# Kernel tuning notes

Hardware: AMD Instinct MI355X
Metric: run time of the kernel (lower is better)

The kernel has to match this reference:

```python
import jax, jax.numpy as jnp
import numpy as np

B, CH, N = 8, 256, 2048


def setup_inputs() -> dict:
    key = jax.random.key(0)
    kk, kq, kv = jax.random.split(key, 3)
    k = jax.random.normal(kk, (B, CH, N), dtype=jnp.float32)
    q = jax.random.normal(kq, (B, N, CH), dtype=jnp.float32)
    v = jax.random.normal(kv, (B, N, CH), dtype=jnp.float32)
    return {"k": k, "q": q, "v": v}


def reference(k, q, v):
    # 'embedded' mode: attn = softmax(ch^-0.5 * q @ k), dropout p=0 is identity
    ch = k.shape[1]
    scale = ch ** (-0.5)
    attn = jax.nn.softmax(scale * jnp.einsum('bnc,bcm->bnm', q, k), axis=-1)  # [B, N, N]
    attended = jnp.einsum('bnm,bmc->bnc', attn, v)  # [B, N, CH]
    return jnp.transpose(attended, (0, 2, 1))  # [B, CH, N]
```

## Files before the change

kernel.cpp:

```cpp
#include <hip/hip_runtime.h>

namespace {

constexpr int kB = 8;
constexpr int kCH = 256;
constexpr int kN = 2048;
constexpr int NSPLIT = 2;
constexpr int SLICE = kN / NSPLIT;
constexpr int KVC = 64;
constexpr int NWAVE = 8;
constexpr int QBLK = 128;
constexpr int PS_STRIDE = KVC + 8;

constexpr float SCALE = 0.0625f;
constexpr float LOG2E = 1.4426950408889634f;
constexpr float DEFER_THR = 4.0f;

typedef _Float16 f16x8 __attribute__((ext_vector_type(8)));
typedef _Float16 f16x4 __attribute__((ext_vector_type(4)));
typedef float f32x4 __attribute__((ext_vector_type(4)));

__device__ __forceinline__ void gload_lds16(const void* g, void* l) {
  __builtin_amdgcn_global_load_lds(
      (const __attribute__((address_space(1))) void*)g,
      (__attribute__((address_space(3))) void*)l, 16, 0, 0);
}

__global__ __launch_bounds__(256) void transpose_both(
    const float* __restrict__ kin, const float* __restrict__ vin,
    _Float16* __restrict__ kt, _Float16* __restrict__ vt) {
  __shared__ _Float16 T[64][72];
  const bool isV = blockIdx.z >= 8;
  const int b = isV ? blockIdx.z - 8 : blockIdx.z;
  const int R = isV ? kN : kCH, C = isV ? kCH : kN;
  const int r0 = (isV ? blockIdx.x : blockIdx.y) * 64;
  const int c0 = (isV ? blockIdx.y : blockIdx.x) * 64;
  const float* in = isV ? vin : kin;
  _Float16* out = isV ? vt : kt;
  const int t = threadIdx.x;

  const float* ib =
      in + (size_t)b * R * C + (size_t)(r0 + (t >> 2)) * C + c0 + (t & 3) * 4;
#pragma unroll
  for (int q = 0; q < 4; ++q) {
    f32x4 v = *(const f32x4*)(ib + q * 16);
    f16x4 w;
    w[0] = (_Float16)v[0]; w[1] = (_Float16)v[1];
    w[2] = (_Float16)v[2]; w[3] = (_Float16)v[3];
    *(f16x4*)(&T[t >> 2][(t & 3) * 4 + q * 16]) = w;
  }
  __syncthreads();
  const int cl = t >> 2, ch = t & 3;
  f16x8 o0, o1;
#pragma unroll
  for (int j = 0; j < 8; ++j) o0[j] = T[ch * 16 + j][cl];
#pragma unroll
  for (int j = 0; j < 8; ++j) o1[j] = T[ch * 16 + 8 + j][cl];
  _Float16* ob = out + (size_t)b * R * C + (size_t)(c0 + cl) * R + r0 + ch * 16;
  *(f16x8*)(ob) = o0;
  *(f16x8*)(ob + 8) = o1;
}

__global__ __launch_bounds__(512, 1) void attn_part(
    const _Float16* __restrict__ kt, const float* __restrict__ qg,
    const _Float16* __restrict__ vt, _Float16* __restrict__ pacc,
    float* __restrict__ pm, float* __restrict__ pl)
{
  __shared__ alignas(16) char KsB[2][64 * 512];
  __shared__ alignas(16) char VsB[2][256 * 128];
  __shared__ alignas(16) _Float16 Ps[NWAVE][16][PS_STRIDE];
  __shared__ float red[NWAVE][16];

  const int tid = threadIdx.x;
  const int wv = tid >> 6;
  const int lane = tid & 63;
  const int s = lane & 15;
  const int qd = lane >> 4;
  const int sw = (s & 7) << 4;
  const int qd16 = qd << 4;

  const int bg = blockIdx.x & 15;
  const int qt = blockIdx.x >> 4;
  const int b = bg >> 1, g = bg & 1;
  const int n0w = qt * QBLK + wv * 16;
  const int kvb = g * SLICE;

  const char* ktB = (const char*)(kt + (size_t)b * kN * kCH);
  const char* vtB = (const char*)(vt + (size_t)b * kCH * kN);
  const float* qb = qg + (size_t)b * kN * kCH;

  f16x8 qf[8];
  {
    const float* qrow = qb + (size_t)(n0w + s) * kCH + qd * 8;
#pragma unroll
    for (int ks = 0; ks < 8; ++ks) {
      f32x4 a = *(const f32x4*)(qrow + ks * 32);
      f32x4 c = *(const f32x4*)(qrow + ks * 32 + 4);
      f16x8 h;
      h[0] = (_Float16)a[0]; h[1] = (_Float16)a[1];
      h[2] = (_Float16)a[2]; h[3] = (_Float16)a[3];
      h[4] = (_Float16)c[0]; h[5] = (_Float16)c[1];
      h[6] = (_Float16)c[2]; h[7] = (_Float16)c[3];
      qf[ks] = h;
    }
  }

  f32x4 acc[16];
#pragma unroll
  for (int i = 0; i < 16; ++i) acc[i] = f32x4{0.f, 0.f, 0.f, 0.f};
  float m_r[4] = {-1e30f, -1e30f, -1e30f, -1e30f};
  float l_r[4] = {0.f, 0.f, 0.f, 0.f};

  auto STAGE = [&](int bf, int kv0) {
    const char* kSrc = ktB + (size_t)kv0 * 512;
    const char* vSrc = vtB + (size_t)kv0 * 2;
    char* kDst = KsB[bf];
    char* vDst = VsB[bf];
#pragma unroll
    for (int ii = 0; ii < 4; ++ii) {
      const int j = ii * 8 + wv;
      const int L = j * 1024 + lane * 16;
      {
        const int row = L >> 9, cb = L & 511;
        gload_lds16(kSrc + (size_t)(row << 9) + (cb ^ ((row & 7) << 4)),
                    kDst + j * 1024);
      }
      {
        const int row = L >> 7, cb = L & 127;
        gload_lds16(vSrc + (size_t)row * 4096 + (cb ^ ((row & 7) << 4)),
                    vDst + j * 1024);
      }
    }
  };

  constexpr int NCHUNK = SLICE / KVC;
  STAGE(0, kvb);
  __syncthreads();

  for (int ck = 0; ck < NCHUNK; ++ck) {
    const int cur = ck & 1;
    if (ck + 1 < NCHUNK) STAGE(cur ^ 1, kvb + (ck + 1) * KVC);

    f32x4 sacc[4];
#pragma unroll
    for (int mc = 0; mc < 4; ++mc) sacc[mc] = f32x4{0.f, 0.f, 0.f, 0.f};
#pragma unroll
    for (int mc = 0; mc < 4; ++mc) {
      const char* kr = KsB[cur] + (mc * 16 + s) * 512;
#pragma unroll
      for (int ks = 0; ks < 8; ++ks) {
        f16x8 bf = *(const f16x8*)(kr + (((ks << 6) | qd16) ^ sw));
        sacc[mc] = __builtin_amdgcn_mfma_f32_16x16x32_f16(qf[ks], bf, sacc[mc], 0, 0, 0);
      }
    }

    float pmax[4];
#pragma unroll
    for (int r = 0; r < 4; ++r)
      pmax[r] = fmaxf(fmaxf(sacc[0][r], sacc[1][r]), fmaxf(sacc[2][r], sacc[3][r]));
#pragma unroll
    for (int off = 1; off < 16; off <<= 1) {
#pragma unroll
      for (int r = 0; r < 4; ++r)
        pmax[r] = fmaxf(pmax[r], __shfl_xor(pmax[r], off, 64));
    }

    bool grow = false;
#pragma unroll
    for (int r = 0; r < 4; ++r)
      grow = grow || (SCALE * pmax[r] > m_r[r] + DEFER_THR);
    if (__any((int)grow)) {
      float corr[4];
#pragma unroll
      for (int r = 0; r < 4; ++r) {
        float mn = fmaxf(m_r[r], SCALE * pmax[r]);
        corr[r] = exp2f((m_r[r] - mn) * LOG2E);
        m_r[r] = mn;
        l_r[r] *= corr[r];
      }
      if (s == 0) {
#pragma unroll
        for (int r = 0; r < 4; ++r) red[wv][qd * 4 + r] = corr[r];
      }
      asm volatile("s_waitcnt lgkmcnt(0)" ::: "memory");
      const float sc = red[wv][s];
#pragma unroll
      for (int i = 0; i < 16; ++i) acc[i] *= sc;
    }

    float lsum[4] = {0.f, 0.f, 0.f, 0.f};
#pragma unroll
    for (int mc = 0; mc < 4; ++mc) {
#pragma unroll
      for (int r = 0; r < 4; ++r) {
        float pvf = exp2f((SCALE * sacc[mc][r] - m_r[r]) * LOG2E);
        lsum[r] += pvf;
        Ps[wv][qd * 4 + r][mc * 16 + s] = (_Float16)pvf;
      }
    }
#pragma unroll
    for (int off = 1; off < 16; off <<= 1) {
#pragma unroll
      for (int r = 0; r < 4; ++r) lsum[r] += __shfl_xor(lsum[r], off, 64);
    }
#pragma unroll
    for (int r = 0; r < 4; ++r) l_r[r] += lsum[r];

    asm volatile("s_waitcnt lgkmcnt(0)" ::: "memory");

#pragma unroll
    for (int ms = 0; ms < 2; ++ms) {
      f16x8 pf = *(const f16x8*)(&Ps[wv][s][ms * 32 + qd * 8]);
#pragma unroll
      for (int ct = 0; ct < 16; ++ct) {
        const char* vr = VsB[cur] + (ct * 16 + s) * 128;
        f16x8 vf = *(const f16x8*)(vr + (((ms << 6) | qd16) ^ sw));
        acc[ct] = __builtin_amdgcn_mfma_f32_16x16x32_f16(vf, pf, acc[ct], 0, 0, 0);
      }
    }
    __syncthreads();
  }

  _Float16* pb = pacc + (size_t)(b * NSPLIT + g) * kCH * kN;
#pragma unroll
  for (int ct = 0; ct < 16; ++ct) {
#pragma unroll
    for (int r = 0; r < 4; ++r) {
      const int c = ct * 16 + qd * 4 + r;
      pb[(size_t)c * kN + n0w + s] = (_Float16)acc[ct][r];
    }
  }
  if (s == 0) {
#pragma unroll
    for (int r = 0; r < 4; ++r) {
      const int n = n0w + qd * 4 + r;
      pm[((size_t)b * kN + n) * NSPLIT + g] = m_r[r];
      pl[((size_t)b * kN + n) * NSPLIT + g] = l_r[r];
    }
  }
}

__global__ void attn_merge(const _Float16* __restrict__ pacc,
                           const float* __restrict__ pm,
                           const float* __restrict__ pl,
                           float* __restrict__ out) {
  const int b = blockIdx.z;
  const int c = blockIdx.y * 16 + (threadIdx.x >> 4);
  const int nn0 = blockIdx.x * 256 + (threadIdx.x & 15) * 16;

  f16x8 dA[NSPLIT], dB[NSPLIT];
#pragma unroll
  for (int g = 0; g < NSPLIT; ++g) {
    const _Float16* p = pacc + ((size_t)(b * NSPLIT + g) * kCH + c) * kN + nn0;
    dA[g] = *(const f16x8*)(p);
    dB[g] = *(const f16x8*)(p + 8);
  }
  float mv[32], lv[32];
  const float* pmB = pm + ((size_t)b * kN + nn0) * NSPLIT;
  const float* plB = pl + ((size_t)b * kN + nn0) * NSPLIT;
#pragma unroll
  for (int q = 0; q < 8; ++q) {
    *(f32x4*)&mv[q * 4] = *(const f32x4*)(pmB + q * 4);
    *(f32x4*)&lv[q * 4] = *(const f32x4*)(plB + q * 4);
  }
  float res[16];
#pragma unroll
  for (int j = 0; j < 16; ++j) {
    float m0 = mv[2 * j], m1 = mv[2 * j + 1];
    float M = fmaxf(m0, m1);
    float a0 = exp2f((m0 - M) * LOG2E);
    float a1 = exp2f((m1 - M) * LOG2E);
    float L = a0 * lv[2 * j] + a1 * lv[2 * j + 1];
    float v = (j < 8) ? a0 * (float)dA[0][j] + a1 * (float)dA[1][j]
                      : a0 * (float)dB[0][j - 8] + a1 * (float)dB[1][j - 8];
    res[j] = v / L;
  }
  float* o = out + ((size_t)b * kCH + c) * kN + nn0;
#pragma unroll
  for (int j = 0; j < 4; ++j)
    *(f32x4*)(o + j * 4) = f32x4{res[j * 4], res[j * 4 + 1], res[j * 4 + 2], res[j * 4 + 3]};
}

constexpr int QBLK_FB = 64;
constexpr int KVBLK_FB = 64;
constexpr int KS_STRIDE_FB = kCH + 8;
constexpr int VS_STRIDE_FB = KVBLK_FB + 8;

__global__ __launch_bounds__(256, 1) void attn_fwd_fb(
    const float* __restrict__ kg, const float* __restrict__ qg,
    const float* __restrict__ vg, float* __restrict__ og)
{
  __shared__ alignas(16) _Float16 Ks[KVBLK_FB][KS_STRIDE_FB];
  __shared__ alignas(16) _Float16 Vs[kCH][VS_STRIDE_FB];
  __shared__ alignas(16) _Float16 Psf[4][16][VS_STRIDE_FB];
  __shared__ float red[4][16];

  const int tid = threadIdx.x;
  const int wv = tid >> 6, lane = tid & 63, s = lane & 15, qd = lane >> 4;
  const int b = blockIdx.x & 7, qt = blockIdx.x >> 3;
  const int n0w = qt * QBLK_FB + wv * 16;
  const float* kb = kg + (size_t)b * kCH * kN;
  const float* qb = qg + (size_t)b * kN * kCH;
  const float* vb = vg + (size_t)b * kN * kCH;
  float* ob = og + (size_t)b * kCH * kN;

  f16x8 qf[8];
  {
    const float* qrow = qb + (size_t)(n0w + s) * kCH + qd * 8;
#pragma unroll
    for (int ks = 0; ks < 8; ++ks) {
      f32x4 a = *(const f32x4*)(qrow + ks * 32);
      f32x4 c = *(const f32x4*)(qrow + ks * 32 + 4);
      f16x8 h;
      h[0] = (_Float16)a[0]; h[1] = (_Float16)a[1];
      h[2] = (_Float16)a[2]; h[3] = (_Float16)a[3];
      h[4] = (_Float16)c[0]; h[5] = (_Float16)c[1];
      h[6] = (_Float16)c[2]; h[7] = (_Float16)c[3];
      qf[ks] = h;
    }
  }
  f32x4 acc[16];
#pragma unroll
  for (int i = 0; i < 16; ++i) acc[i] = f32x4{0.f, 0.f, 0.f, 0.f};
  float m_r[4] = {-1e30f, -1e30f, -1e30f, -1e30f};
  float l_r[4] = {0.f, 0.f, 0.f, 0.f};

  for (int kv0 = 0; kv0 < kN; kv0 += KVBLK_FB) {
    __syncthreads();
    {
      const int m0 = 4 * (tid >> 4), c0b = 4 * (tid & 15);
#pragma unroll
      for (int p = 0; p < 4; ++p) {
        const int c0 = c0b + 64 * p;
        const float* src = kb + (size_t)c0 * kN + kv0 + m0;
        f32x4 r0 = *(const f32x4*)(src);
        f32x4 r1 = *(const f32x4*)(src + kN);
        f32x4 r2 = *(const f32x4*)(src + 2 * kN);
        f32x4 r3 = *(const f32x4*)(src + 3 * kN);
#pragma unroll
        for (int i = 0; i < 4; ++i) {
          f16x4 w;
          w[0] = (_Float16)r0[i]; w[1] = (_Float16)r1[i];
          w[2] = (_Float16)r2[i]; w[3] = (_Float16)r3[i];
          *(f16x4*)(&Ks[m0 + i][c0]) = w;
        }
      }
    }
    {
      const int m0 = 4 * (tid & 15), c0b = 4 * (tid >> 4);
#pragma unroll
      for (int p = 0; p < 4; ++p) {
        const int c0 = c0b + 64 * p;
        const float* src = vb + (size_t)(kv0 + m0) * kCH + c0;
        f32x4 r0 = *(const f32x4*)(src);
        f32x4 r1 = *(const f32x4*)(src + kCH);
        f32x4 r2 = *(const f32x4*)(src + 2 * kCH);
        f32x4 r3 = *(const f32x4*)(src + 3 * kCH);
#pragma unroll
        for (int i = 0; i < 4; ++i) {
          f16x4 w;
          w[0] = (_Float16)r0[i]; w[1] = (_Float16)r1[i];
          w[2] = (_Float16)r2[i]; w[3] = (_Float16)r3[i];
          *(f16x4*)(&Vs[c0 + i][m0]) = w;
        }
      }
    }
    __syncthreads();

    f32x4 sacc[4];
#pragma unroll
    for (int mc = 0; mc < 4; ++mc) sacc[mc] = f32x4{0.f, 0.f, 0.f, 0.f};
#pragma unroll
    for (int mc = 0; mc < 4; ++mc) {
#pragma unroll
      for (int ks = 0; ks < 8; ++ks) {
        f16x8 bf = *(const f16x8*)(&Ks[mc * 16 + s][ks * 32 + qd * 8]);
        sacc[mc] = __builtin_amdgcn_mfma_f32_16x16x32_f16(qf[ks], bf, sacc[mc], 0, 0, 0);
      }
    }
    float pmax[4];
#pragma unroll
    for (int r = 0; r < 4; ++r)
      pmax[r] = fmaxf(fmaxf(sacc[0][r], sacc[1][r]), fmaxf(sacc[2][r], sacc[3][r]));
#pragma unroll
    for (int off = 1; off < 16; off <<= 1) {
#pragma unroll
      for (int r = 0; r < 4; ++r)
        pmax[r] = fmaxf(pmax[r], __shfl_xor(pmax[r], off, 64));
    }
    float corr[4], lsum[4];
#pragma unroll
    for (int r = 0; r < 4; ++r) {
      float mn = fmaxf(m_r[r], SCALE * pmax[r]);
      corr[r] = exp2f((m_r[r] - mn) * LOG2E);
      m_r[r] = mn;
      lsum[r] = 0.f;
    }
#pragma unroll
    for (int mc = 0; mc < 4; ++mc) {
#pragma unroll
      for (int r = 0; r < 4; ++r) {
        float pvf = exp2f((SCALE * sacc[mc][r] - m_r[r]) * LOG2E);
        lsum[r] += pvf;
        Psf[wv][qd * 4 + r][mc * 16 + s] = (_Float16)pvf;
      }
    }
#pragma unroll
    for (int off = 1; off < 16; off <<= 1) {
#pragma unroll
      for (int r = 0; r < 4; ++r) lsum[r] += __shfl_xor(lsum[r], off, 64);
    }
#pragma unroll
    for (int r = 0; r < 4; ++r) l_r[r] = l_r[r] * corr[r] + lsum[r];
    if (s == 0) {
#pragma unroll
      for (int r = 0; r < 4; ++r) red[wv][qd * 4 + r] = corr[r];
    }
    asm volatile("s_waitcnt lgkmcnt(0)" ::: "memory");
    const float sc = red[wv][s];
#pragma unroll
    for (int i = 0; i < 16; ++i) acc[i] *= sc;
#pragma unroll
    for (int ms = 0; ms < 2; ++ms) {
      f16x8 pf = *(const f16x8*)(&Psf[wv][s][ms * 32 + qd * 8]);
#pragma unroll
      for (int ct = 0; ct < 16; ++ct) {
        f16x8 vf = *(const f16x8*)(&Vs[ct * 16 + s][ms * 32 + qd * 8]);
        acc[ct] = __builtin_amdgcn_mfma_f32_16x16x32_f16(vf, pf, acc[ct], 0, 0, 0);
      }
    }
  }
  if (s == 0) {
#pragma unroll
    for (int r = 0; r < 4; ++r) red[wv][qd * 4 + r] = 1.0f / l_r[r];
  }
  asm volatile("s_waitcnt lgkmcnt(0)" ::: "memory");
  const float inv = red[wv][s];
#pragma unroll
  for (int ct = 0; ct < 16; ++ct) {
#pragma unroll
    for (int r = 0; r < 4; ++r) {
      const int c = ct * 16 + qd * 4 + r;
      ob[(size_t)c * kN + n0w + s] = acc[ct][r] * inv;
    }
  }
}

constexpr size_t KT_ELEMS = (size_t)kB * kN * kCH;
constexpr size_t PACC_ELEMS = (size_t)NSPLIT * kB * kCH * kN;
constexpr size_t PM_ELEMS = (size_t)kB * kN * NSPLIT;
constexpr size_t WS_NEED =
    (2 * KT_ELEMS + PACC_ELEMS) * sizeof(_Float16) + 2 * PM_ELEMS * sizeof(float);

}

extern "C" void kernel_launch(void* const* d_in, const int* in_sizes, int n_in,
                              void* d_out, int out_size, void* d_ws, size_t ws_size,
                              hipStream_t stream) {
  (void)in_sizes; (void)n_in; (void)out_size;
  const float* k = (const float*)d_in[0];
  const float* q = (const float*)d_in[1];
  const float* v = (const float*)d_in[2];
  float* out = (float*)d_out;

  if (ws_size < WS_NEED) {
    hipLaunchKernelGGL(attn_fwd_fb, dim3(kB * (kN / QBLK_FB)), dim3(256), 0, stream,
                       k, q, v, out);
    return;
  }

  _Float16* kt = (_Float16*)d_ws;
  _Float16* vt = kt + KT_ELEMS;
  _Float16* pacc = vt + KT_ELEMS;
  float* pm = (float*)(pacc + PACC_ELEMS);
  float* pl = pm + PM_ELEMS;

  hipLaunchKernelGGL(transpose_both, dim3(kN / 64, kCH / 64, 16), dim3(256), 0,
                     stream, k, v, kt, vt);
  hipLaunchKernelGGL(attn_part, dim3(kB * (kN / QBLK) * NSPLIT), dim3(512), 0,
                     stream, kt, q, vt, pacc, pm, pl);
  hipLaunchKernelGGL(attn_merge, dim3(kN / 256, kCH / 16, kB), dim3(256), 0, stream,
                     pacc, pm, pl, out);
}
```

Before: 174.1 us.

## Switch attention to 32x32 MFMA with register-resident P and four-way KV split

Rewrites the main attention kernel around 32x32x16 MFMA tiles. Each wave now owns 32 query rows, and S is computed transposed so the P tile stays in registers, repacked with cvt_pkrtz and permlane32_swap instead of being staged through LDS. The KV dimension is split four ways and blocks are allowed two per CU, and the merge kernel now combines four partials. The transpose kernel drops its shared-memory stage and writes f16x4 directly. The aim is to remove the LDS round trip for P and the cross-lane reductions and to raise occupancy, at the cost of more register pressure and more partial-output traffic.

```diff
diff --git a/kernel.cpp b/kernel.cpp
--- a/kernel.cpp
+++ b/kernel.cpp
@@ -1,24 +1,26 @@
 #include <hip/hip_runtime.h>
+#include <stdint.h>
 
 namespace {
 
 constexpr int kB = 8;
 constexpr int kCH = 256;
 constexpr int kN = 2048;
-constexpr int NSPLIT = 2;
+constexpr int NSPLIT = 4;
 constexpr int SLICE = kN / NSPLIT;
 constexpr int KVC = 64;
-constexpr int NWAVE = 8;
-constexpr int QBLK = 128;
-constexpr int PS_STRIDE = KVC + 8;
+constexpr int NCHUNK = SLICE / KVC;
+constexpr int QBLK = 256;
 
 constexpr float SCALE = 0.0625f;
 constexpr float LOG2E = 1.4426950408889634f;
-constexpr float DEFER_THR = 4.0f;
+constexpr float THR = 4.0f;
 
 typedef _Float16 f16x8 __attribute__((ext_vector_type(8)));
 typedef _Float16 f16x4 __attribute__((ext_vector_type(4)));
 typedef float f32x4 __attribute__((ext_vector_type(4)));
+typedef float f32x16 __attribute__((ext_vector_type(16)));
+typedef unsigned int u32x4 __attribute__((ext_vector_type(4)));
 
 __device__ __forceinline__ void gload_lds16(const void* g, void* l) {
   __builtin_amdgcn_global_load_lds(
@@ -29,65 +31,267 @@
 __global__ __launch_bounds__(256) void transpose_both(
     const float* __restrict__ kin, const float* __restrict__ vin,
     _Float16* __restrict__ kt, _Float16* __restrict__ vt) {
-  __shared__ _Float16 T[64][72];
   const bool isV = blockIdx.z >= 8;
-  const int b = isV ? blockIdx.z - 8 : blockIdx.z;
+  const int b = isV ? (int)blockIdx.z - 8 : (int)blockIdx.z;
   const int R = isV ? kN : kCH, C = isV ? kCH : kN;
-  const int r0 = (isV ? blockIdx.x : blockIdx.y) * 64;
-  const int c0 = (isV ? blockIdx.y : blockIdx.x) * 64;
+  const int r0 = (isV ? (int)blockIdx.x : (int)blockIdx.y) * 64;
+  const int c0 = (isV ? (int)blockIdx.y : (int)blockIdx.x) * 64;
   const float* in = isV ? vin : kin;
   _Float16* out = isV ? vt : kt;
   const int t = threadIdx.x;
-
-  const float* ib =
-      in + (size_t)b * R * C + (size_t)(r0 + (t >> 2)) * C + c0 + (t & 3) * 4;
-#pragma unroll
-  for (int q = 0; q < 4; ++q) {
-    f32x4 v = *(const f32x4*)(ib + q * 16);
+  const int rr = 4 * (t >> 4), cc = 4 * (t & 15);
+  const float* src = in + (size_t)b * R * C + (size_t)(r0 + rr) * C + c0 + cc;
+  f32x4 v0 = *(const f32x4*)(src);
+  f32x4 v1 = *(const f32x4*)(src + (size_t)C);
+  f32x4 v2 = *(const f32x4*)(src + 2 * (size_t)C);
+  f32x4 v3 = *(const f32x4*)(src + 3 * (size_t)C);
+  _Float16* ob = out + (size_t)b * R * C + r0 + rr;
+#pragma unroll
+  for (int j = 0; j < 4; ++j) {
     f16x4 w;
-    w[0] = (_Float16)v[0]; w[1] = (_Float16)v[1];
-    w[2] = (_Float16)v[2]; w[3] = (_Float16)v[3];
-    *(f16x4*)(&T[t >> 2][(t & 3) * 4 + q * 16]) = w;
-  }
-  __syncthreads();
-  const int cl = t >> 2, ch = t & 3;
-  f16x8 o0, o1;
-#pragma unroll
-  for (int j = 0; j < 8; ++j) o0[j] = T[ch * 16 + j][cl];
-#pragma unroll
-  for (int j = 0; j < 8; ++j) o1[j] = T[ch * 16 + 8 + j][cl];
-  _Float16* ob = out + (size_t)b * R * C + (size_t)(c0 + cl) * R + r0 + ch * 16;
-  *(f16x8*)(ob) = o0;
-  *(f16x8*)(ob + 8) = o1;
-}
-
-__global__ __launch_bounds__(512, 1) void attn_part(
+    w[0] = (_Float16)v0[j]; w[1] = (_Float16)v1[j];
+    w[2] = (_Float16)v2[j]; w[3] = (_Float16)v3[j];
+    *(f16x4*)(ob + (size_t)(c0 + cc + j) * R) = w;
+  }
+}
+
+__global__ __launch_bounds__(512, 2) void attn_part(
     const _Float16* __restrict__ kt, const float* __restrict__ qg,
     const _Float16* __restrict__ vt, _Float16* __restrict__ pacc,
     float* __restrict__ pm, float* __restrict__ pl)
 {
   __shared__ alignas(16) char KsB[2][64 * 512];
   __shared__ alignas(16) char VsB[2][256 * 128];
-  __shared__ alignas(16) _Float16 Ps[NWAVE][16][PS_STRIDE];
-  __shared__ float red[NWAVE][16];
 
   const int tid = threadIdx.x;
   const int wv = tid >> 6;
   const int lane = tid & 63;
-  const int s = lane & 15;
-  const int qd = lane >> 4;
-  const int sw = (s & 7) << 4;
-  const int qd16 = qd << 4;
-
-  const int bg = blockIdx.x & 15;
-  const int qt = blockIdx.x >> 4;
-  const int b = bg >> 1, g = bg & 1;
-  const int n0w = qt * QBLK + wv * 16;
+  const int lq = lane & 31;
+  const int hi = lane >> 5;
+
+  const int bg = blockIdx.x & 31;
+  const int qt = blockIdx.x >> 5;
+  const int b = bg >> 2, g = bg & 3;
+  const int n0w = qt * QBLK + wv * 32;
   const int kvb = g * SLICE;
 
   const char* ktB = (const char*)(kt + (size_t)b * kN * kCH);
   const char* vtB = (const char*)(vt + (size_t)b * kCH * kN);
   const float* qb = qg + (size_t)b * kN * kCH;
+
+  f16x8 qf[16];
+  {
+    const float* qrow = qb + (size_t)(n0w + lq) * kCH + 8 * hi;
+#pragma unroll
+    for (int kq = 0; kq < 16; ++kq) {
+      f32x4 a = *(const f32x4*)(qrow + 16 * kq);
+      f32x4 c = *(const f32x4*)(qrow + 16 * kq + 4);
+      f16x8 h;
+      h[0] = (_Float16)a[0]; h[1] = (_Float16)a[1];
+      h[2] = (_Float16)a[2]; h[3] = (_Float16)a[3];
+      h[4] = (_Float16)c[0]; h[5] = (_Float16)c[1];
+      h[6] = (_Float16)c[2]; h[7] = (_Float16)c[3];
+      qf[kq] = h;
+    }
+  }
+
+  f32x16 acc[8];
+#pragma unroll
+  for (int i = 0; i < 8; ++i) {
+#pragma unroll
+    for (int j = 0; j < 16; ++j) acc[i][j] = 0.f;
+  }
+  float m_r = -1e30f, l_r = 0.f;
+
+  auto STAGE = [&](int bf, int kv0) {
+    const char* kSrc = ktB + (size_t)kv0 * 512;
+    const char* vSrc = vtB + (size_t)kv0 * 2;
+    char* kDst = KsB[bf];
+    char* vDst = VsB[bf];
+#pragma unroll
+    for (int ii = 0; ii < 4; ++ii) {
+      const int j = ii * 8 + wv;
+      const int L = j * 1024 + lane * 16;
+      {
+        const int row = L >> 9, cb = L & 511;
+        gload_lds16(kSrc + (size_t)(row << 9) + (cb ^ ((row & 7) << 4)),
+                    kDst + j * 1024);
+      }
+      {
+        const int row = L >> 7, cb = L & 127;
+        gload_lds16(vSrc + (size_t)row * 4096 + (cb ^ ((row & 7) << 4)),
+                    vDst + j * 1024);
+      }
+    }
+  };
+
+  STAGE(0, kvb);
+  __syncthreads();
+
+  for (int ck = 0; ck < NCHUNK; ++ck) {
+    const int cur = ck & 1;
+    if (ck + 1 < NCHUNK) STAGE(cur ^ 1, kvb + (ck + 1) * KVC);
+
+#pragma unroll
+    for (int t = 0; t < 2; ++t) {
+      f32x16 sacc;
+#pragma unroll
+      for (int j = 0; j < 16; ++j) sacc[j] = 0.f;
+      const int krow = t * 32 + lq;
+      const char* kr = KsB[cur] + krow * 512;
+      const int swk = (krow & 7) << 4;
+#pragma unroll
+      for (int kq = 0; kq < 16; ++kq) {
+        f16x8 af = *(const f16x8*)(kr + ((32 * kq + 16 * hi) ^ swk));
+        sacc = __builtin_amdgcn_mfma_f32_32x32x16_f16(af, qf[kq], sacc, 0, 0, 0);
+      }
+
+      float t8[8];
+#pragma unroll
+      for (int j = 0; j < 8; ++j) t8[j] = fmaxf(sacc[2 * j], sacc[2 * j + 1]);
+      float t4a = fmaxf(fmaxf(t8[0], t8[1]), fmaxf(t8[2], t8[3]));
+      float t4b = fmaxf(fmaxf(t8[4], t8[5]), fmaxf(t8[6], t8[7]));
+      float mx = fmaxf(t4a, t4b);
+      mx = fmaxf(mx, __shfl_xor(mx, 32, 64));
+
+      bool grow = (SCALE * mx > m_r + THR);
+      if (__any((int)grow)) {
+        float mn = fmaxf(m_r, SCALE * mx);
+        float corr = exp2f((m_r - mn) * LOG2E);
+        m_r = mn;
+        l_r *= corr;
+#pragma unroll
+        for (int i = 0; i < 8; ++i) {
+#pragma unroll
+          for (int j = 0; j < 16; ++j) acc[i][j] *= corr;
+        }
+      }
+
+      float p[16];
+      const float kSL = SCALE * LOG2E;
+      const float mb = -m_r * LOG2E;
+#pragma unroll
+      for (int r = 0; r < 16; ++r) p[r] = exp2f(fmaf(sacc[r], kSL, mb));
+      float s8[8];
+#pragma unroll
+      for (int j = 0; j < 8; ++j) s8[j] = p[2 * j] + p[2 * j + 1];
+      float ls = ((s8[0] + s8[1]) + (s8[2] + s8[3])) +
+                 ((s8[4] + s8[5]) + (s8[6] + s8[7]));
+      ls += __shfl_xor(ls, 32, 64);
+      l_r += ls;
+
+#pragma unroll
+      for (int ks = 0; ks < 2; ++ks) {
+        auto x0 = __builtin_amdgcn_cvt_pkrtz(p[8 * ks + 0], p[8 * ks + 1]);
+        auto x1 = __builtin_amdgcn_cvt_pkrtz(p[8 * ks + 2], p[8 * ks + 3]);
+        auto x2 = __builtin_amdgcn_cvt_pkrtz(p[8 * ks + 4], p[8 * ks + 5]);
+        auto x3 = __builtin_amdgcn_cvt_pkrtz(p[8 * ks + 6], p[8 * ks + 7]);
+        uint32_t a0 = __builtin_bit_cast(uint32_t, x0);
+        uint32_t a1 = __builtin_bit_cast(uint32_t, x1);
+        uint32_t a2 = __builtin_bit_cast(uint32_t, x2);
+        uint32_t a3 = __builtin_bit_cast(uint32_t, x3);
+        asm("v_permlane32_swap_b32 %0, %1" : "+v"(a0), "+v"(a2));
+        asm("v_permlane32_swap_b32 %0, %1" : "+v"(a1), "+v"(a3));
+        u32x4 w; w[0] = a0; w[1] = a1; w[2] = a2; w[3] = a3;
+        f16x8 pf = __builtin_bit_cast(f16x8, w);
+
+        const int vOff = 64 * t + 32 * ks + 16 * hi;
+#pragma unroll
+        for (int ct = 0; ct < 8; ++ct) {
+          const int vrow = ct * 32 + lq;
+          f16x8 vf = *(const f16x8*)(VsB[cur] + vrow * 128 +
+                                     (vOff ^ ((vrow & 7) << 4)));
+          acc[ct] = __builtin_amdgcn_mfma_f32_32x32x16_f16(vf, pf, acc[ct], 0, 0, 0);
+        }
+      }
+    }
+    __syncthreads();
+  }
+
+  _Float16* pb = pacc + (size_t)(b * NSPLIT + g) * kCH * kN + n0w + lq;
+#pragma unroll
+  for (int ct = 0; ct < 8; ++ct) {
+#pragma unroll
+    for (int r = 0; r < 16; ++r) {
+      const int c = ct * 32 + (r & 3) + 8 * (r >> 2) + 4 * hi;
+      pb[(size_t)c * kN] = (_Float16)acc[ct][r];
+    }
+  }
+  if (lane < 32) {
+    const int n = n0w + lane;
+    pm[((size_t)b * kN + n) * NSPLIT + g] = m_r;
+    pl[((size_t)b * kN + n) * NSPLIT + g] = l_r;
+  }
+}
+
+__global__ void attn_merge(const _Float16* __restrict__ pacc,
+                           const float* __restrict__ pm,
+                           const float* __restrict__ pl,
+                           float* __restrict__ out) {
+  const int b = blockIdx.z;
+  const int c = blockIdx.y * 16 + ((int)threadIdx.x >> 4);
+  const int nn0 = blockIdx.x * 256 + ((int)threadIdx.x & 15) * 16;
+
+  const float* pmB = pm + ((size_t)b * kN + nn0) * NSPLIT;
+  const float* plB = pl + ((size_t)b * kN + nn0) * NSPLIT;
+  float res[16];
+
+#pragma unroll
+  for (int h = 0; h < 2; ++h) {
+    float mv[32], lv[32];
+#pragma unroll
+    for (int q = 0; q < 8; ++q) {
+      *(f32x4*)&mv[q * 4] = *(const f32x4*)(pmB + h * 32 + q * 4);
+      *(f32x4*)&lv[q * 4] = *(const f32x4*)(plB + h * 32 + q * 4);
+    }
+    f16x8 d[NSPLIT];
+#pragma unroll
+    for (int g = 0; g < NSPLIT; ++g)
+      d[g] = *(const f16x8*)(pacc + ((size_t)(b * NSPLIT + g) * kCH + c) * kN +
+                             nn0 + h * 8);
+#pragma unroll
+    for (int j = 0; j < 8; ++j) {
+      float m0 = mv[4 * j], m1 = mv[4 * j + 1], m2 = mv[4 * j + 2], m3 = mv[4 * j + 3];
+      float M = fmaxf(fmaxf(m0, m1), fmaxf(m2, m3));
+      float a0 = exp2f((m0 - M) * LOG2E);
+      float a1 = exp2f((m1 - M) * LOG2E);
+      float a2 = exp2f((m2 - M) * LOG2E);
+      float a3 = exp2f((m3 - M) * LOG2E);
+      float L = a0 * lv[4 * j] + a1 * lv[4 * j + 1] + a2 * lv[4 * j + 2] +
+                a3 * lv[4 * j + 3];
+      float v = a0 * (float)d[0][j] + a1 * (float)d[1][j] +
+                a2 * (float)d[2][j] + a3 * (float)d[3][j];
+      res[h * 8 + j] = v / L;
+    }
+  }
+  float* o = out + ((size_t)b * kCH + c) * kN + nn0;
+#pragma unroll
+  for (int j = 0; j < 4; ++j)
+    *(f32x4*)(o + j * 4) = f32x4{res[j * 4], res[j * 4 + 1], res[j * 4 + 2], res[j * 4 + 3]};
+}
+
+constexpr int QBLK_FB = 64;
+constexpr int KVBLK_FB = 64;
+constexpr int KS_STRIDE_FB = kCH + 8;
+constexpr int VS_STRIDE_FB = KVBLK_FB + 8;
+
+__global__ __launch_bounds__(256, 1) void attn_fwd_fb(
+    const float* __restrict__ kg, const float* __restrict__ qg,
+    const float* __restrict__ vg, float* __restrict__ og)
+{
+  __shared__ alignas(16) _Float16 Ks[KVBLK_FB][KS_STRIDE_FB];
+  __shared__ alignas(16) _Float16 Vs[kCH][VS_STRIDE_FB];
+  __shared__ alignas(16) _Float16 Psf[4][16][VS_STRIDE_FB];
+  __shared__ float red[4][16];
+
+  const int tid = threadIdx.x;
+  const int wv = tid >> 6, lane = tid & 63, s = lane & 15, qd = lane >> 4;
+  const int b = blockIdx.x & 7, qt = blockIdx.x >> 3;
+  const int n0w = qt * QBLK_FB + wv * 16;
+  const float* kb = kg + (size_t)b * kCH * kN;
+  const float* qb = qg + (size_t)b * kN * kCH;
+  const float* vb = vg + (size_t)b * kN * kCH;
+  float* ob = og + (size_t)b * kCH * kN;
 
   f16x8 qf[8];
   {
@@ -104,221 +308,6 @@
       qf[ks] = h;
     }
   }
-
-  f32x4 acc[16];
-#pragma unroll
-  for (int i = 0; i < 16; ++i) acc[i] = f32x4{0.f, 0.f, 0.f, 0.f};
-  float m_r[4] = {-1e30f, -1e30f, -1e30f, -1e30f};
-  float l_r[4] = {0.f, 0.f, 0.f, 0.f};
-
-  auto STAGE = [&](int bf, int kv0) {
-    const char* kSrc = ktB + (size_t)kv0 * 512;
-    const char* vSrc = vtB + (size_t)kv0 * 2;
-    char* kDst = KsB[bf];
-    char* vDst = VsB[bf];
-#pragma unroll
-    for (int ii = 0; ii < 4; ++ii) {
-      const int j = ii * 8 + wv;
-      const int L = j * 1024 + lane * 16;
-      {
-        const int row = L >> 9, cb = L & 511;
-        gload_lds16(kSrc + (size_t)(row << 9) + (cb ^ ((row & 7) << 4)),
-                    kDst + j * 1024);
-      }
-      {
-        const int row = L >> 7, cb = L & 127;
-        gload_lds16(vSrc + (size_t)row * 4096 + (cb ^ ((row & 7) << 4)),
-                    vDst + j * 1024);
-      }
-    }
-  };
-
-  constexpr int NCHUNK = SLICE / KVC;
-  STAGE(0, kvb);
-  __syncthreads();
-
-  for (int ck = 0; ck < NCHUNK; ++ck) {
-    const int cur = ck & 1;
-    if (ck + 1 < NCHUNK) STAGE(cur ^ 1, kvb + (ck + 1) * KVC);
-
-    f32x4 sacc[4];
-#pragma unroll
-    for (int mc = 0; mc < 4; ++mc) sacc[mc] = f32x4{0.f, 0.f, 0.f, 0.f};
-#pragma unroll
-    for (int mc = 0; mc < 4; ++mc) {
-      const char* kr = KsB[cur] + (mc * 16 + s) * 512;
-#pragma unroll
-      for (int ks = 0; ks < 8; ++ks) {
-        f16x8 bf = *(const f16x8*)(kr + (((ks << 6) | qd16) ^ sw));
-        sacc[mc] = __builtin_amdgcn_mfma_f32_16x16x32_f16(qf[ks], bf, sacc[mc], 0, 0, 0);
-      }
-    }
-
-    float pmax[4];
-#pragma unroll
-    for (int r = 0; r < 4; ++r)
-      pmax[r] = fmaxf(fmaxf(sacc[0][r], sacc[1][r]), fmaxf(sacc[2][r], sacc[3][r]));
-#pragma unroll
-    for (int off = 1; off < 16; off <<= 1) {
-#pragma unroll
-      for (int r = 0; r < 4; ++r)
-        pmax[r] = fmaxf(pmax[r], __shfl_xor(pmax[r], off, 64));
-    }
-
-    bool grow = false;
-#pragma unroll
-    for (int r = 0; r < 4; ++r)
-      grow = grow || (SCALE * pmax[r] > m_r[r] + DEFER_THR);
-    if (__any((int)grow)) {
-      float corr[4];
-#pragma unroll
-      for (int r = 0; r < 4; ++r) {
-        float mn = fmaxf(m_r[r], SCALE * pmax[r]);
-        corr[r] = exp2f((m_r[r] - mn) * LOG2E);
-        m_r[r] = mn;
-        l_r[r] *= corr[r];
-      }
-      if (s == 0) {
-#pragma unroll
-        for (int r = 0; r < 4; ++r) red[wv][qd * 4 + r] = corr[r];
-      }
-      asm volatile("s_waitcnt lgkmcnt(0)" ::: "memory");
-      const float sc = red[wv][s];
-#pragma unroll
-      for (int i = 0; i < 16; ++i) acc[i] *= sc;
-    }
-
-    float lsum[4] = {0.f, 0.f, 0.f, 0.f};
-#pragma unroll
-    for (int mc = 0; mc < 4; ++mc) {
-#pragma unroll
-      for (int r = 0; r < 4; ++r) {
-        float pvf = exp2f((SCALE * sacc[mc][r] - m_r[r]) * LOG2E);
-        lsum[r] += pvf;
-        Ps[wv][qd * 4 + r][mc * 16 + s] = (_Float16)pvf;
-      }
-    }
-#pragma unroll
-    for (int off = 1; off < 16; off <<= 1) {
-#pragma unroll
-      for (int r = 0; r < 4; ++r) lsum[r] += __shfl_xor(lsum[r], off, 64);
-    }
-#pragma unroll
-    for (int r = 0; r < 4; ++r) l_r[r] += lsum[r];
-
-    asm volatile("s_waitcnt lgkmcnt(0)" ::: "memory");
-
-#pragma unroll
-    for (int ms = 0; ms < 2; ++ms) {
-      f16x8 pf = *(const f16x8*)(&Ps[wv][s][ms * 32 + qd * 8]);
-#pragma unroll
-      for (int ct = 0; ct < 16; ++ct) {
-        const char* vr = VsB[cur] + (ct * 16 + s) * 128;
-        f16x8 vf = *(const f16x8*)(vr + (((ms << 6) | qd16) ^ sw));
-        acc[ct] = __builtin_amdgcn_mfma_f32_16x16x32_f16(vf, pf, acc[ct], 0, 0, 0);
-      }
-    }
-    __syncthreads();
-  }
-
-  _Float16* pb = pacc + (size_t)(b * NSPLIT + g) * kCH * kN;
-#pragma unroll
-  for (int ct = 0; ct < 16; ++ct) {
-#pragma unroll
-    for (int r = 0; r < 4; ++r) {
-      const int c = ct * 16 + qd * 4 + r;
-      pb[(size_t)c * kN + n0w + s] = (_Float16)acc[ct][r];
-    }
-  }
-  if (s == 0) {
-#pragma unroll
-    for (int r = 0; r < 4; ++r) {
-      const int n = n0w + qd * 4 + r;
-      pm[((size_t)b * kN + n) * NSPLIT + g] = m_r[r];
-      pl[((size_t)b * kN + n) * NSPLIT + g] = l_r[r];
-    }
-  }
-}
-
-__global__ void attn_merge(const _Float16* __restrict__ pacc,
-                           const float* __restrict__ pm,
-                           const float* __restrict__ pl,
-                           float* __restrict__ out) {
-  const int b = blockIdx.z;
-  const int c = blockIdx.y * 16 + (threadIdx.x >> 4);
-  const int nn0 = blockIdx.x * 256 + (threadIdx.x & 15) * 16;
-
-  f16x8 dA[NSPLIT], dB[NSPLIT];
-#pragma unroll
-  for (int g = 0; g < NSPLIT; ++g) {
-    const _Float16* p = pacc + ((size_t)(b * NSPLIT + g) * kCH + c) * kN + nn0;
-    dA[g] = *(const f16x8*)(p);
-    dB[g] = *(const f16x8*)(p + 8);
-  }
-  float mv[32], lv[32];
-  const float* pmB = pm + ((size_t)b * kN + nn0) * NSPLIT;
-  const float* plB = pl + ((size_t)b * kN + nn0) * NSPLIT;
-#pragma unroll
-  for (int q = 0; q < 8; ++q) {
-    *(f32x4*)&mv[q * 4] = *(const f32x4*)(pmB + q * 4);
-    *(f32x4*)&lv[q * 4] = *(const f32x4*)(plB + q * 4);
-  }
-  float res[16];
-#pragma unroll
-  for (int j = 0; j < 16; ++j) {
-    float m0 = mv[2 * j], m1 = mv[2 * j + 1];
-    float M = fmaxf(m0, m1);
-    float a0 = exp2f((m0 - M) * LOG2E);
-    float a1 = exp2f((m1 - M) * LOG2E);
-    float L = a0 * lv[2 * j] + a1 * lv[2 * j + 1];
-    float v = (j < 8) ? a0 * (float)dA[0][j] + a1 * (float)dA[1][j]
-                      : a0 * (float)dB[0][j - 8] + a1 * (float)dB[1][j - 8];
-    res[j] = v / L;
-  }
-  float* o = out + ((size_t)b * kCH + c) * kN + nn0;
-#pragma unroll
-  for (int j = 0; j < 4; ++j)
-    *(f32x4*)(o + j * 4) = f32x4{res[j * 4], res[j * 4 + 1], res[j * 4 + 2], res[j * 4 + 3]};
-}
-
-constexpr int QBLK_FB = 64;
-constexpr int KVBLK_FB = 64;
-constexpr int KS_STRIDE_FB = kCH + 8;
-constexpr int VS_STRIDE_FB = KVBLK_FB + 8;
-
-__global__ __launch_bounds__(256, 1) void attn_fwd_fb(
-    const float* __restrict__ kg, const float* __restrict__ qg,
-    const float* __restrict__ vg, float* __restrict__ og)
-{
-  __shared__ alignas(16) _Float16 Ks[KVBLK_FB][KS_STRIDE_FB];
-  __shared__ alignas(16) _Float16 Vs[kCH][VS_STRIDE_FB];
-  __shared__ alignas(16) _Float16 Psf[4][16][VS_STRIDE_FB];
-  __shared__ float red[4][16];
-
-  const int tid = threadIdx.x;
-  const int wv = tid >> 6, lane = tid & 63, s = lane & 15, qd = lane >> 4;
-  const int b = blockIdx.x & 7, qt = blockIdx.x >> 3;
-  const int n0w = qt * QBLK_FB + wv * 16;
-  const float* kb = kg + (size_t)b * kCH * kN;
-  const float* qb = qg + (size_t)b * kN * kCH;
-  const float* vb = vg + (size_t)b * kN * kCH;
-  float* ob = og + (size_t)b * kCH * kN;
-
-  f16x8 qf[8];
-  {
-    const float* qrow = qb + (size_t)(n0w + s) * kCH + qd * 8;
-#pragma unroll
-    for (int ks = 0; ks < 8; ++ks) {
-      f32x4 a = *(const f32x4*)(qrow + ks * 32);
-      f32x4 c = *(const f32x4*)(qrow + ks * 32 + 4);
-      f16x8 h;
-      h[0] = (_Float16)a[0]; h[1] = (_Float16)a[1];
-      h[2] = (_Float16)a[2]; h[3] = (_Float16)a[3];
-      h[4] = (_Float16)c[0]; h[5] = (_Float16)c[1];
-      h[6] = (_Float16)c[2]; h[7] = (_Float16)c[3];
-      qf[ks] = h;
-    }
-  }
   f32x4 acc[16];
 #pragma unroll
   for (int i = 0; i < 16; ++i) acc[i] = f32x4{0.f, 0.f, 0.f, 0.f};
```

Result: slower. 184.7 us (+6.1%).
